# Kernel tuning notes

Measured on AMD Instinct MI355X. Metric: run time of the kernel, lower is better.

The kernel has to match this reference:

```python
import jax, jax.numpy as jnp
import numpy as np

WH, WW = 12, 12
NUM_HEADS = 8
NW = 4


def _relative_position_index():
    ch, cw = np.meshgrid(np.arange(WH), np.arange(WW), indexing='ij')
    coords = np.stack([ch, cw]).reshape(2, -1)            # [2, Wh*Ww]
    rel = coords[:, :, None] - coords[:, None, :]         # [2, M, M]
    rel = rel.transpose(1, 2, 0)                          # [M, M, 2]
    rel[:, :, 0] += WH - 1
    rel[:, :, 1] += WW - 1
    rel[:, :, 0] *= 2 * WW - 1
    return jnp.asarray(rel.sum(-1))                       # [M, M] int


def setup_inputs() -> dict:
    key = jax.random.key(0)
    ks = jax.random.split(key, 11)
    C = 512
    B_, N = 512, WH * WW + 1
    std = 0.02
    return {
        'x': jax.random.normal(ks[0], (B_, N, C), dtype=jnp.float32),
        'mask': jnp.zeros((NW, N, N), dtype=jnp.float32),
        'rpb_table': jax.random.normal(ks[1], ((2 * WH - 1) * (2 * WW - 1), NUM_HEADS), dtype=jnp.float32) * std,
        'Wq': jax.random.normal(ks[2], (C, C), dtype=jnp.float32) * (C ** -0.5),
        'bq': jax.random.normal(ks[3], (C,), dtype=jnp.float32) * std,
        'Wk': jax.random.normal(ks[4], (C, C), dtype=jnp.float32) * (C ** -0.5),
        'bk': jax.random.normal(ks[5], (C,), dtype=jnp.float32) * std,
        'Wv': jax.random.normal(ks[6], (C, C), dtype=jnp.float32) * (C ** -0.5),
        'bv': jax.random.normal(ks[7], (C,), dtype=jnp.float32) * std,
        'Wo': jax.random.normal(ks[8], (C, C), dtype=jnp.float32) * (C ** -0.5),
        'bo': jax.random.normal(ks[9], (C,), dtype=jnp.float32) * std,
    }


def reference(x, mask, rpb_table, Wq, bq, Wk, bk, Wv, bv, Wo, bo):
    B_, N, C = x.shape
    H = NUM_HEADS
    hd = C // H
    scale = hd ** -0.5
    B = B_ // NW
    M = WH * WW  # window tokens (N = M + 1 global token)

    def proj(W, b):
        return (x @ W.T + b).reshape(B_, N, H, hd).transpose(0, 2, 1, 3)  # [B_,H,N,hd]

    q = proj(Wq, bq)
    k = proj(Wk, bk)
    v = proj(Wv, bv)

    attn = jnp.einsum('bhnd,bhmd->bhnm', q, k) * scale  # [B_,H,N,N]

    rel_idx = _relative_position_index()                 # [M,M]
    bias = rpb_table[rel_idx].transpose(2, 0, 1)          # [H,M,M]
    attn = attn.at[:, :, :M, :M].add(bias[None])          # N != M: bias on window block only

    # shifted-window mask: (nW, N, N)
    attn = (attn.reshape(B, NW, H, N, N) + mask[None, :, None]).reshape(B_, H, N, N)

    # ---- global-token attention redistribution (gx) ----
    ga = attn[:, :, -1, :].reshape(B, NW, H, N).transpose(0, 2, 1, 3)   # [B,H,NW,N]
    g1 = ga[:, :, :, :M].reshape(B, H, NW * M)                           # window keys, all windows
    g2 = ga[:, :, :, M].mean(-1, keepdims=True)                          # mean global-global logit [B,H,1]
    g = jax.nn.softmax(jnp.concatenate([g1, g2], axis=-1), axis=-1)      # [B,H,NW*M+1]
    g1 = g[:, :, :-1].reshape(B, H, NW, M).transpose(0, 2, 1, 3).reshape(B_, H, M)
    g2 = jnp.broadcast_to(g[:, :, -1][:, None, :], (B, NW, H)).reshape(B_, H, 1)
    ga_full = jnp.concatenate([g1, g2], axis=-1)[:, :, None, :]          # [B_,H,1,N]
    gx = jnp.einsum('bhqn,bhnd->bhqd', ga_full, v).transpose(0, 2, 1, 3).reshape(B_, C)
    gx = gx.reshape(B, NW, C).sum(1)                                     # sum over windows [B,C]
    gx = jnp.broadcast_to(gx[:, None, :], (B, NW, C)).reshape(B_, C)

    # ---- standard window attention ----
    attn = jax.nn.softmax(attn, axis=-1)
    out = jnp.einsum('bhnm,bhmd->bhnd', attn, v).transpose(0, 2, 1, 3).reshape(B_, N, C)
    out = out.at[:, -1, :].set(gx)
    return out @ Wo.T + bo
```

## Files before the change

kernel.cpp:

```cpp
#include <hip/hip_runtime.h>
#include <hip/hip_bf16.h>
#include <stdint.h>

#define NTOK 145
#define MTOK 144
#define CDIM 512
#define NHEAD 8
#define HD 64
#define NWIN 4
#define BWIN 512
#define MROWS (BWIN*NTOK)

typedef short short8 __attribute__((ext_vector_type(8)));
typedef float f32x4 __attribute__((ext_vector_type(4)));

__device__ __forceinline__ uint16_t f2bf(float f) {
  union { float f; uint32_t u; } x; x.f = f;
  uint32_t r = x.u + 0x7FFFu + ((x.u >> 16) & 1u);
  return (uint16_t)(r >> 16);
}
__device__ __forceinline__ float bf2f(uint16_t u) {
  union { uint32_t u; float f; } x; x.u = ((uint32_t)u) << 16; return x.f;
}
__device__ __forceinline__ uint32_t pack2(float a, float b) {
  return (uint32_t)f2bf(a) | ((uint32_t)f2bf(b) << 16);
}

#define GLL(gp, lp) __builtin_amdgcn_global_load_lds( \
    (const __attribute__((address_space(1))) uint32_t*)(gp), \
    (__attribute__((address_space(3))) uint32_t*)(lp), 16, 0, 0)

__global__ __launch_bounds__(256) void cast_x(const float* __restrict__ x,
                                              uint16_t* __restrict__ xb) {
  size_t id = ((size_t)blockIdx.x*256 + threadIdx.x)*8;
  float4 a = *(const float4*)(x+id), c = *(const float4*)(x+id+4);
  uint4 o = make_uint4(pack2(a.x,a.y), pack2(a.z,a.w), pack2(c.x,c.y), pack2(c.z,c.w));
  *(uint4*)(xb+id) = o;
}

__global__ void prep_kernel(const float* __restrict__ rpb,
                            const float* __restrict__ Wq, const float* __restrict__ bq,
                            const float* __restrict__ Wk, const float* __restrict__ bk,
                            const float* __restrict__ Wv, const float* __restrict__ bv,
                            const float* __restrict__ Wo, const float* __restrict__ mask,
                            uint16_t* __restrict__ wqkv, uint16_t* __restrict__ wo,
                            float* __restrict__ bqkv, float* __restrict__ ltab) {
  int id = blockIdx.x * 256 + threadIdx.x;
  const int A = 1536*512, B = 512*512, C2 = 1536, E = 4*8*145*160;
  if (id < A) {
    int n = id >> 9, k = id & 511;
    const float* W = (n < 512) ? Wq : (n < 1024) ? Wk : Wv;
    wqkv[id] = f2bf(W[(size_t)(n & 511)*512 + k]);
  } else if ((id -= A) < B) {
    wo[id] = f2bf(Wo[id]);
  } else if ((id -= B) < C2) {
    bqkv[id] = (id < 512) ? bq[id] : (id < 1024) ? bk[id-512] : bv[id-1024];
  } else if ((id -= C2) < E) {
    int nw = id / (8*145*160);
    int r2 = id % (8*145*160);
    int h = r2 / (145*160);
    int r3 = r2 % (145*160);
    int i = r3 / 160, j = r3 % 160;
    float v = 0.f;
    if (j < 145) v = mask[(nw*145 + i)*145 + j];
    if (i < 144 && j < 144) {
      int rel = (i/12 - j/12 + 11) * 23 + (i%12 - j%12 + 11);
      v += rpb[rel*8 + h];
    }
    ltab[id] = v;
  }
}

__global__ __launch_bounds__(512, 2) void gemm_qkv(
    const uint16_t* __restrict__ xb, const uint16_t* __restrict__ wqkv,
    const float* __restrict__ bqkv,
    uint16_t* __restrict__ qb, uint16_t* __restrict__ kb, uint16_t* __restrict__ vb) {
  __shared__ __align__(16) uint16_t As[4*256*32];
  __shared__ __align__(16) uint16_t Bs[4*256*32];
  int bid = blockIdx.x;
  int mb, nb;
  if (bid < 1728) { int g = bid / 48, r = bid % 48; mb = g*8 + (r & 7); nb = r >> 3; }
  else            { int r = bid - 1728;             mb = 288 + (r & 1); nb = r >> 1; }
  int tid = threadIdx.x, lane = tid & 63, w = tid >> 6;
  int wm = w >> 2, wn = w & 3;
  int lm = lane & 15, lq = lane >> 4;

  int srow = lane >> 2, scol = (lane & 3) * 8;
  const uint16_t* agp = xb   + (size_t)(mb*256 + w*32 + srow)*512 + scol;
  const uint16_t* bgp = wqkv + (size_t)(nb*256 + w*32 + srow)*512 + scol;

  f32x4 acc[8][4];
#pragma unroll
  for (int a = 0; a < 8; a++)
#pragma unroll
    for (int b = 0; b < 4; b++) acc[a][b] = (f32x4){0.f,0.f,0.f,0.f};

  #define STAGE_QKV(slot, kt) { \
    uint16_t* Ad = &As[(slot)*8192 + (w*32)*32]; \
    uint16_t* Bd = &Bs[(slot)*8192 + (w*32)*32]; \
    GLL(agp + (kt)*32,           Ad); \
    GLL(agp + (kt)*32 + 16*512,  Ad + 16*32); \
    GLL(bgp + (kt)*32,           Bd); \
    GLL(bgp + (kt)*32 + 16*512,  Bd + 16*32); \
  }

  #define COMPUTE_QKV(slot) { \
    const uint16_t* Ab = &As[(slot)*8192 + (wm*128 + lm)*32 + lq*8]; \
    const uint16_t* Bb = &Bs[(slot)*8192 + (wn*64  + lm)*32 + lq*8]; \
    short8 a[8], b[4]; \
    _Pragma("unroll") \
    for (int mr = 0; mr < 8; mr++) a[mr] = *(const short8*)&Ab[mr*16*32]; \
    _Pragma("unroll") \
    for (int nr = 0; nr < 4; nr++) b[nr] = *(const short8*)&Bb[nr*16*32]; \
    __builtin_amdgcn_s_setprio(1); \
    _Pragma("unroll") \
    for (int mr = 0; mr < 8; mr++) \
      _Pragma("unroll") \
      for (int nr = 0; nr < 4; nr++) \
        acc[mr][nr] = __builtin_amdgcn_mfma_f32_16x16x32_bf16(a[mr], b[nr], acc[mr][nr], 0, 0, 0); \
    __builtin_amdgcn_s_setprio(0); \
  }

  STAGE_QKV(0, 0);
  STAGE_QKV(1, 1);
  for (int kt = 0; kt < 15; kt++) {
    asm volatile("s_waitcnt vmcnt(4)" ::: "memory");
    __builtin_amdgcn_s_barrier();
    __builtin_amdgcn_sched_barrier(0);
    if (kt < 14) STAGE_QKV((kt + 2) & 3, kt + 2);
    COMPUTE_QKV(kt & 3);
  }
  asm volatile("s_waitcnt vmcnt(0)" ::: "memory");
  __builtin_amdgcn_s_barrier();
  __builtin_amdgcn_sched_barrier(0);
  COMPUTE_QKV(3);

  #undef STAGE_QKV
  #undef COMPUTE_QKV

#pragma unroll
  for (int nr = 0; nr < 4; nr++) {
    int n = nb*256 + wn*64 + nr*16 + lm;
    float bias = bqkv[n];
    int which = nb >> 1;
    uint16_t* dst = (which == 0) ? qb : (which == 1) ? kb : vb;
    int c = n & 511;
    int hh = c >> 6, dd = c & 63;
#pragma unroll
    for (int mr = 0; mr < 8; mr++) {
#pragma unroll
      for (int r = 0; r < 4; r++) {
        int m = mb*256 + wm*128 + mr*16 + lq*4 + r;
        int bw = m / 145, nl = m - bw*145;
        dst[((size_t)(bw*8 + hh)*145 + nl)*64 + dd] = f2bf(acc[mr][nr][r] + bias);
      }
    }
  }
}

__global__ __launch_bounds__(256, 3) void attn_kernel(
    const uint16_t* __restrict__ qb, const uint16_t* __restrict__ kb,
    const uint16_t* __restrict__ vb, const float* __restrict__ ltab,
    float* __restrict__ glog, uint16_t* __restrict__ attn_out) {
  __shared__ __align__(16) uint16_t P[80*168];
  __shared__ __align__(16) uint16_t vt[64*168];
  int bid = blockIdx.x;
  int half = bid & 1;
  int h = (bid >> 1) & 7;
  int b_ = bid >> 4;
  int nw = b_ & 3;
  int tid = threadIdx.x, lane = tid & 63, w = tid >> 6;
  int lm = lane & 15, lq = lane >> 4;
  const size_t hbase = ((size_t)(b_*8 + h)) * (145*64);
  const uint16_t* qp = qb + hbase;
  const uint16_t* kp = kb + hbase;
  const uint16_t* vp = vb + hbase;
  const float* ltp = ltab + (size_t)(nw*8 + h)*(145*160);

  for (int c = tid; c < 1160; c += 256) {
    int j = c >> 3, d0 = (c & 7) * 8;
    uint16_t tmp[8];
    *(uint4*)tmp = *(const uint4*)(vp + (size_t)j*64 + d0);
#pragma unroll
    for (int t = 0; t < 8; t++) vt[(d0 + t)*168 + j] = tmp[t];
  }
  for (int c = tid; c < 960; c += 256)
    vt[(c/15)*168 + 145 + (c%15)] = 0;

  for (int ltile = w; ltile < 5; ltile += 4) {
    int gt = half*5 + ltile;
    f32x4 acc[10];
#pragma unroll
    for (int nt = 0; nt < 10; nt++) {
#pragma unroll
      for (int r = 0; r < 4; r++) {
        int i = gt*16 + lq*4 + r; if (i > 144) i = 144;
        acc[nt][r] = 8.0f * ltp[i*160 + nt*16 + lm];
      }
    }
    int iq = gt*16 + lm; if (iq > 144) iq = 144;
#pragma unroll
    for (int ks = 0; ks < 2; ks++) {
      short8 afr = *(const short8*)(qp + (size_t)iq*64 + ks*32 + lq*8);
#pragma unroll
      for (int nt = 0; nt < 10; nt++) {
        int j = nt*16 + lm; if (j > 144) j = 144;
        short8 bfr = *(const short8*)(kp + (size_t)j*64 + ks*32 + lq*8);
        acc[nt] = __builtin_amdgcn_mfma_f32_16x16x32_bf16(afr, bfr, acc[nt], 0, 0, 0);
      }
    }
    if (gt == 9) {
      if (lq == 0) {
#pragma unroll
        for (int nt = 0; nt < 10; nt++) {
          int j = nt*16 + lm;
          if (j < 145)
            glog[(size_t)(b_*8 + h)*145 + j] = acc[nt][0]*0.125f;
        }
      }
    } else {
#pragma unroll
      for (int r = 0; r < 4; r++) {
        int prow = ltile*16 + lq*4 + r;
        float mx = -3.0e38f;
#pragma unroll
        for (int nt = 0; nt < 10; nt++) {
          int j = nt*16 + lm;
          float t = acc[nt][r]*0.125f;
          if (j >= 145) t = -3.0e38f;
          acc[nt][r] = t;
          mx = fmaxf(mx, t);
        }
#pragma unroll
        for (int off = 1; off < 16; off <<= 1) mx = fmaxf(mx, __shfl_xor(mx, off));
        float sum = 0.f;
#pragma unroll
        for (int nt = 0; nt < 10; nt++) {
          int j = nt*16 + lm;
          float p = (j < 145) ? __expf(acc[nt][r] - mx) : 0.f;
          acc[nt][r] = p; sum += p;
        }
#pragma unroll
        for (int off = 1; off < 16; off <<= 1) sum += __shfl_xor(sum, off);
        float rs = __builtin_amdgcn_rcpf(sum);
#pragma unroll
        for (int nt = 0; nt < 10; nt++)
          P[prow*168 + nt*16 + lm] = f2bf(acc[nt][r] * rs);
      }
    }
  }
  __syncthreads();

  int npv = 5 - half;
  f32x4 oacc[5];
#pragma unroll
  for (int mt = 0; mt < 5; mt++) oacc[mt] = (f32x4){0.f,0.f,0.f,0.f};
#pragma unroll
  for (int ks = 0; ks < 5; ks++) {
    short8 bfr = *(const short8*)&vt[(w*16 + lm)*168 + ks*32 + lq*8];
#pragma unroll
    for (int mt = 0; mt < 5; mt++) {
      if (mt < npv) {
        short8 afr = *(const short8*)&P[(mt*16 + lm)*168 + ks*32 + lq*8];
        oacc[mt] = __builtin_amdgcn_mfma_f32_16x16x32_bf16(afr, bfr, oacc[mt], 0, 0, 0);
      }
    }
  }
#pragma unroll
  for (int mt = 0; mt < 5; mt++) {
    if (mt < npv) {
#pragma unroll
      for (int r = 0; r < 4; r++) {
        int i = half*80 + mt*16 + lq*4 + r;
        attn_out[((size_t)b_*145 + i)*512 + h*64 + w*16 + lm] = f2bf(oacc[mt][r]);
      }
    }
  }
}

__global__ __launch_bounds__(256) void gx_kernel(
    const float* __restrict__ glog, const uint16_t* __restrict__ vb,
    uint16_t* __restrict__ attn_out) {
  int bid = blockIdx.x;
  int b = bid >> 3, h = bid & 7;
  int tid = threadIdx.x, lane = tid & 63, w = tid >> 6;
  __shared__ float lg[580];
  __shared__ float pl[576];
  __shared__ float sred[8];
  __shared__ float sacc[256];
  for (int t = tid; t < 580; t += 256) {
    int nwi = t / 145, j = t - nwi*145;
    lg[t] = glog[(size_t)((b*4 + nwi)*8 + h)*145 + j];
  }
  __syncthreads();
  float g2 = 0.25f*(lg[144] + lg[289] + lg[434] + lg[579]);
  float mx = g2;
  for (int t = tid; t < 576; t += 256) {
    int nwi = t / 144, j = t - nwi*144;
    mx = fmaxf(mx, lg[nwi*145 + j]);
  }
#pragma unroll
  for (int off = 1; off < 64; off <<= 1) mx = fmaxf(mx, __shfl_xor(mx, off));
  if (lane == 0) sred[w] = mx;
  __syncthreads();
  mx = fmaxf(fmaxf(sred[0], sred[1]), fmaxf(sred[2], sred[3]));
  float sum = 0.f;
  for (int t = tid; t < 576; t += 256) {
    int nwi = t / 144, j = t - nwi*144;
    float p = __expf(lg[nwi*145 + j] - mx);
    pl[t] = p; sum += p;
  }
#pragma unroll
  for (int off = 1; off < 64; off <<= 1) sum += __shfl_xor(sum, off);
  if (lane == 0) sred[4 + w] = sum;
  __syncthreads();
  sum = (sred[4] + sred[5]) + (sred[6] + sred[7]);
  float p2 = __expf(g2 - mx);
  float rs = __builtin_amdgcn_rcpf(sum + p2);
  const uint16_t* vp = vb + (size_t)((b*4 + w)*8 + h)*(145*64);
  float acc = 0.f;
  int d = lane;
#pragma unroll 4
  for (int j = 0; j < 144; j++)
    acc += pl[w*144 + j] * bf2f(vp[j*64 + d]);
  acc += p2 * bf2f(vp[144*64 + d]);
  sacc[tid] = acc;
  __syncthreads();
  if (w == 0) {
    float tot = (sacc[lane] + sacc[64 + lane]) + (sacc[128 + lane] + sacc[192 + lane]);
    uint16_t o = f2bf(tot * rs);
    for (int nwi = 0; nwi < 4; nwi++)
      attn_out[((size_t)(b*4 + nwi)*145 + 144)*512 + h*64 + d] = o;
  }
}

__global__ __launch_bounds__(512, 2) void gemm_out(
    const uint16_t* __restrict__ A, const uint16_t* __restrict__ wo,
    const float* __restrict__ bo, float* __restrict__ out) {
  __shared__ __align__(16) uint16_t As[4*256*32];
  __shared__ __align__(16) uint16_t Bs[4*256*32];
  int bid = blockIdx.x;
  int mb, nb;
  if (bid < 576) { int g = bid / 16, r = bid % 16; mb = g*8 + (r & 7); nb = r >> 3; }
  else           { int r = bid - 576;              mb = 288 + (r & 1); nb = r >> 1; }
  int tid = threadIdx.x, lane = tid & 63, w = tid >> 6;
  int wm = w >> 2, wn = w & 3;
  int lm = lane & 15, lq = lane >> 4;

  int srow = lane >> 2, scol = (lane & 3) * 8;
  const uint16_t* agp = A  + (size_t)(mb*256 + w*32 + srow)*512 + scol;
  const uint16_t* bgp = wo + (size_t)(nb*256 + w*32 + srow)*512 + scol;

  f32x4 acc[8][4];
#pragma unroll
  for (int a = 0; a < 8; a++)
#pragma unroll
    for (int b = 0; b < 4; b++) acc[a][b] = (f32x4){0.f,0.f,0.f,0.f};

  #define STAGE_O(slot, kt) { \
    uint16_t* Ad = &As[(slot)*8192 + (w*32)*32]; \
    uint16_t* Bd = &Bs[(slot)*8192 + (w*32)*32]; \
    GLL(agp + (kt)*32,           Ad); \
    GLL(agp + (kt)*32 + 16*512,  Ad + 16*32); \
    GLL(bgp + (kt)*32,           Bd); \
    GLL(bgp + (kt)*32 + 16*512,  Bd + 16*32); \
  }

  #define COMPUTE_O(slot) { \
    const uint16_t* Ab = &As[(slot)*8192 + (wm*128 + lm)*32 + lq*8]; \
    const uint16_t* Bb = &Bs[(slot)*8192 + (wn*64  + lm)*32 + lq*8]; \
    short8 a[8], b[4]; \
    _Pragma("unroll") \
    for (int mr = 0; mr < 8; mr++) a[mr] = *(const short8*)&Ab[mr*16*32]; \
    _Pragma("unroll") \
    for (int nr = 0; nr < 4; nr++) b[nr] = *(const short8*)&Bb[nr*16*32]; \
    __builtin_amdgcn_s_setprio(1); \
    _Pragma("unroll") \
    for (int mr = 0; mr < 8; mr++) \
      _Pragma("unroll") \
      for (int nr = 0; nr < 4; nr++) \
        acc[mr][nr] = __builtin_amdgcn_mfma_f32_16x16x32_bf16(a[mr], b[nr], acc[mr][nr], 0, 0, 0); \
    __builtin_amdgcn_s_setprio(0); \
  }

  STAGE_O(0, 0);
  STAGE_O(1, 1);
  for (int kt = 0; kt < 15; kt++) {
    asm volatile("s_waitcnt vmcnt(4)" ::: "memory");
    __builtin_amdgcn_s_barrier();
    __builtin_amdgcn_sched_barrier(0);
    if (kt < 14) STAGE_O((kt + 2) & 3, kt + 2);
    COMPUTE_O(kt & 3);
  }
  asm volatile("s_waitcnt vmcnt(0)" ::: "memory");
  __builtin_amdgcn_s_barrier();
  __builtin_amdgcn_sched_barrier(0);
  COMPUTE_O(3);

  #undef STAGE_O
  #undef COMPUTE_O

#pragma unroll
  for (int nr = 0; nr < 4; nr++) {
    int n = nb*256 + wn*64 + nr*16 + lm;
    float bias = bo[n];
#pragma unroll
    for (int mr = 0; mr < 8; mr++) {
#pragma unroll
      for (int r = 0; r < 4; r++) {
        int m = mb*256 + wm*128 + mr*16 + lq*4 + r;
        out[(size_t)m*512 + n] = acc[mr][nr][r] + bias;
      }
    }
  }
}

extern "C" void kernel_launch(void* const* d_in, const int* in_sizes, int n_in,
                              void* d_out, int out_size, void* d_ws, size_t ws_size,
                              hipStream_t stream) {
  const float* x    = (const float*)d_in[0];
  const float* mask = (const float*)d_in[1];
  const float* rpb  = (const float*)d_in[2];
  const float* Wq   = (const float*)d_in[3];
  const float* bq   = (const float*)d_in[4];
  const float* Wk   = (const float*)d_in[5];
  const float* bk   = (const float*)d_in[6];
  const float* Wv   = (const float*)d_in[7];
  const float* bv   = (const float*)d_in[8];
  const float* Wo   = (const float*)d_in[9];
  const float* bo   = (const float*)d_in[10];

  uint8_t* ws = (uint8_t*)d_ws;
  size_t off = 0;
  auto alloc = [&](size_t bytes) -> void* {
    void* p = ws + off; off += (bytes + 255) & ~(size_t)255; return p;
  };
  uint16_t* wqkv   = (uint16_t*)alloc((size_t)1536*512*2);
  uint16_t* wo     = (uint16_t*)alloc((size_t)512*512*2);
  float*    bqkv   = (float*)alloc(1536*4);
  float*    ltab   = (float*)alloc((size_t)4*8*145*160*4);
  float*    glog   = (float*)alloc((size_t)512*8*145*4);
  uint16_t* xb     = (uint16_t*)alloc((size_t)MROWS*512*2);
  uint16_t* qb     = (uint16_t*)alloc((size_t)MROWS*512*2);
  uint16_t* kb     = (uint16_t*)alloc((size_t)MROWS*512*2);
  uint16_t* vb     = (uint16_t*)alloc((size_t)MROWS*512*2);
  uint16_t* attn   = (uint16_t*)alloc((size_t)MROWS*512*2);

  cast_x<<<18560, 256, 0, stream>>>(x, xb);
  prep_kernel<<<7002, 256, 0, stream>>>(rpb, Wq, bq, Wk, bk, Wv, bv, Wo, mask,
                                        wqkv, wo, bqkv, ltab);
  gemm_qkv<<<1740, 512, 0, stream>>>(xb, wqkv, bqkv, qb, kb, vb);
  attn_kernel<<<8192, 256, 0, stream>>>(qb, kb, vb, ltab, glog, attn);
  gx_kernel<<<1024, 256, 0, stream>>>(glog, vb, attn);
  gemm_out<<<580, 512, 0, stream>>>(attn, wo, bo, (float*)d_out);
}
```

Before: 728.3 us.

## Swizzle LDS tiles and transpose MFMA operands for vectorized GEMM epilogues

Both projection GEMMs now feed the weight tile as the MFMA A operand and the activation tile as B. Each lane's accumulator then holds four consecutive output columns, so the epilogue can issue packed bf16 (uint2) or float4 stores plus float4 bias loads instead of scalar stores. The LDS layout gains an XOR swizzle on the 8-element chunk index, applied to both the global-to-LDS staging and the fragment reads, to reduce bank conflicts. The swizzle has to match exactly between writer and reader, and the warp tile shape changes from 128x64 to 64 rows by 128 columns.

```diff
diff --git a/kernel.cpp b/kernel.cpp
--- a/kernel.cpp
+++ b/kernel.cpp
@@ -82,12 +82,15 @@
   if (bid < 1728) { int g = bid / 48, r = bid % 48; mb = g*8 + (r & 7); nb = r >> 3; }
   else            { int r = bid - 1728;             mb = 288 + (r & 1); nb = r >> 1; }
   int tid = threadIdx.x, lane = tid & 63, w = tid >> 6;
-  int wm = w >> 2, wn = w & 3;
+  int wnA = w >> 2;
+  int wmB = w & 3;
   int lm = lane & 15, lq = lane >> 4;
 
-  int srow = lane >> 2, scol = (lane & 3) * 8;
-  const uint16_t* agp = xb   + (size_t)(mb*256 + w*32 + srow)*512 + scol;
-  const uint16_t* bgp = wqkv + (size_t)(nb*256 + w*32 + srow)*512 + scol;
+  int srow = lane >> 2;
+  int schunk = (lane & 3) ^ ((lane >> 3) & 3);
+  const uint16_t* agp = xb   + (size_t)(mb*256 + w*32 + srow)*512 + schunk*8;
+  const uint16_t* bgp = wqkv + (size_t)(nb*256 + w*32 + srow)*512 + schunk*8;
+  int rc = (lq ^ ((lm >> 1) & 3)) * 8;
 
   f32x4 acc[8][4];
 #pragma unroll
@@ -105,19 +108,19 @@
   }
 
   #define COMPUTE_QKV(slot) { \
-    const uint16_t* Ab = &As[(slot)*8192 + (wm*128 + lm)*32 + lq*8]; \
-    const uint16_t* Bb = &Bs[(slot)*8192 + (wn*64  + lm)*32 + lq*8]; \
-    short8 a[8], b[4]; \
-    _Pragma("unroll") \
-    for (int mr = 0; mr < 8; mr++) a[mr] = *(const short8*)&Ab[mr*16*32]; \
-    _Pragma("unroll") \
-    for (int nr = 0; nr < 4; nr++) b[nr] = *(const short8*)&Bb[nr*16*32]; \
+    const uint16_t* Wb = &Bs[(slot)*8192 + (wnA*128 + lm)*32 + rc]; \
+    const uint16_t* Xb = &As[(slot)*8192 + (wmB*64  + lm)*32 + rc]; \
+    short8 wf[8], xf[4]; \
+    _Pragma("unroll") \
+    for (int na = 0; na < 8; na++) wf[na] = *(const short8*)&Wb[na*16*32]; \
+    _Pragma("unroll") \
+    for (int mt = 0; mt < 4; mt++) xf[mt] = *(const short8*)&Xb[mt*16*32]; \
     __builtin_amdgcn_s_setprio(1); \
     _Pragma("unroll") \
-    for (int mr = 0; mr < 8; mr++) \
+    for (int na = 0; na < 8; na++) \
       _Pragma("unroll") \
-      for (int nr = 0; nr < 4; nr++) \
-        acc[mr][nr] = __builtin_amdgcn_mfma_f32_16x16x32_bf16(a[mr], b[nr], acc[mr][nr], 0, 0, 0); \
+      for (int mt = 0; mt < 4; mt++) \
+        acc[na][mt] = __builtin_amdgcn_mfma_f32_16x16x32_bf16(wf[na], xf[mt], acc[na][mt], 0, 0, 0); \
     __builtin_amdgcn_s_setprio(0); \
   }
 
@@ -138,22 +141,28 @@
   #undef STAGE_QKV
   #undef COMPUTE_QKV
 
-#pragma unroll
-  for (int nr = 0; nr < 4; nr++) {
-    int n = nb*256 + wn*64 + nr*16 + lm;
-    float bias = bqkv[n];
-    int which = nb >> 1;
-    uint16_t* dst = (which == 0) ? qb : (which == 1) ? kb : vb;
-    int c = n & 511;
-    int hh = c >> 6, dd = c & 63;
-#pragma unroll
-    for (int mr = 0; mr < 8; mr++) {
-#pragma unroll
-      for (int r = 0; r < 4; r++) {
-        int m = mb*256 + wm*128 + mr*16 + lq*4 + r;
-        int bw = m / 145, nl = m - bw*145;
-        dst[((size_t)(bw*8 + hh)*145 + nl)*64 + dd] = f2bf(acc[mr][nr][r] + bias);
-      }
+  int which = nb >> 1;
+  uint16_t* dst = (which == 0) ? qb : (which == 1) ? kb : vb;
+#pragma unroll
+  for (int mt = 0; mt < 4; mt++) {
+    int m = mb*256 + wmB*64 + mt*16 + lm;
+    int bw = m / 145, nl = m - bw*145;
+    size_t mbase = (size_t)bw*8*9280 + (size_t)nl*64;
+#pragma unroll
+    for (int na = 0; na < 8; na++) {
+      int n0 = nb*256 + wnA*128 + na*16 + lq*4;
+      float4 b4 = *(const float4*)&bqkv[n0];
+      int c = n0 & 511;
+      int hh = c >> 6, d0 = c & 63;
+      float f0 = acc[na][mt][0] + b4.x;
+      float f1 = acc[na][mt][1] + b4.y;
+      float f2 = acc[na][mt][2] + b4.z;
+      float f3 = acc[na][mt][3] + b4.w;
+      uint32_t lo, hi;
+      asm("v_cvt_pk_bf16_f32 %0, %1, %2" : "=v"(lo) : "v"(f0), "v"(f1));
+      asm("v_cvt_pk_bf16_f32 %0, %1, %2" : "=v"(hi) : "v"(f2), "v"(f3));
+      uint2 pk; pk.x = lo; pk.y = hi;
+      *(uint2*)(dst + mbase + (size_t)hh*9280 + d0) = pk;
     }
   }
 }
@@ -344,12 +353,15 @@
   if (bid < 576) { int g = bid / 16, r = bid % 16; mb = g*8 + (r & 7); nb = r >> 3; }
   else           { int r = bid - 576;              mb = 288 + (r & 1); nb = r >> 1; }
   int tid = threadIdx.x, lane = tid & 63, w = tid >> 6;
-  int wm = w >> 2, wn = w & 3;
+  int wnA = w >> 2;
+  int wmB = w & 3;
   int lm = lane & 15, lq = lane >> 4;
 
-  int srow = lane >> 2, scol = (lane & 3) * 8;
-  const uint16_t* agp = A  + (size_t)(mb*256 + w*32 + srow)*512 + scol;
-  const uint16_t* bgp = wo + (size_t)(nb*256 + w*32 + srow)*512 + scol;
+  int srow = lane >> 2;
+  int schunk = (lane & 3) ^ ((lane >> 3) & 3);
+  const uint16_t* agp = A  + (size_t)(mb*256 + w*32 + srow)*512 + schunk*8;
+  const uint16_t* bgp = wo + (size_t)(nb*256 + w*32 + srow)*512 + schunk*8;
+  int rc = (lq ^ ((lm >> 1) & 3)) * 8;
 
   f32x4 acc[8][4];
 #pragma unroll
@@ -367,19 +379,19 @@
   }
 
   #define COMPUTE_O(slot) { \
-    const uint16_t* Ab = &As[(slot)*8192 + (wm*128 + lm)*32 + lq*8]; \
-    const uint16_t* Bb = &Bs[(slot)*8192 + (wn*64  + lm)*32 + lq*8]; \
-    short8 a[8], b[4]; \
-    _Pragma("unroll") \
-    for (int mr = 0; mr < 8; mr++) a[mr] = *(const short8*)&Ab[mr*16*32]; \
-    _Pragma("unroll") \
-    for (int nr = 0; nr < 4; nr++) b[nr] = *(const short8*)&Bb[nr*16*32]; \
+    const uint16_t* Wb = &Bs[(slot)*8192 + (wnA*128 + lm)*32 + rc]; \
+    const uint16_t* Xb = &As[(slot)*8192 + (wmB*64  + lm)*32 + rc]; \
+    short8 wf[8], xf[4]; \
+    _Pragma("unroll") \
+    for (int na = 0; na < 8; na++) wf[na] = *(const short8*)&Wb[na*16*32]; \
+    _Pragma("unroll") \
+    for (int mt = 0; mt < 4; mt++) xf[mt] = *(const short8*)&Xb[mt*16*32]; \
     __builtin_amdgcn_s_setprio(1); \
     _Pragma("unroll") \
-    for (int mr = 0; mr < 8; mr++) \
+    for (int na = 0; na < 8; na++) \
       _Pragma("unroll") \
-      for (int nr = 0; nr < 4; nr++) \
-        acc[mr][nr] = __builtin_amdgcn_mfma_f32_16x16x32_bf16(a[mr], b[nr], acc[mr][nr], 0, 0, 0); \
+      for (int mt = 0; mt < 4; mt++) \
+        acc[na][mt] = __builtin_amdgcn_mfma_f32_16x16x32_bf16(wf[na], xf[mt], acc[na][mt], 0, 0, 0); \
     __builtin_amdgcn_s_setprio(0); \
   }
 
@@ -401,16 +413,19 @@
   #undef COMPUTE_O
 
 #pragma unroll
-  for (int nr = 0; nr < 4; nr++) {
-    int n = nb*256 + wn*64 + nr*16 + lm;
-    float bias = bo[n];
-#pragma unroll
-    for (int mr = 0; mr < 8; mr++) {
-#pragma unroll
-      for (int r = 0; r < 4; r++) {
-        int m = mb*256 + wm*128 + mr*16 + lq*4 + r;
-        out[(size_t)m*512 + n] = acc[mr][nr][r] + bias;
-      }
+  for (int mt = 0; mt < 4; mt++) {
+    int m = mb*256 + wmB*64 + mt*16 + lm;
+    float* orow = out + (size_t)m*512;
+#pragma unroll
+    for (int na = 0; na < 8; na++) {
+      int n0 = nb*256 + wnA*128 + na*16 + lq*4;
+      float4 b4 = *(const float4*)&bo[n0];
+      float4 o;
+      o.x = acc[na][mt][0] + b4.x;
+      o.y = acc[na][mt][1] + b4.y;
+      o.z = acc[na][mt][2] + b4.z;
+      o.w = acc[na][mt][3] + b4.w;
+      *(float4*)(orow + n0) = o;
     }
   }
 }
```

After: 720.1 us. Within noise of the previous version (-1.1%).
